# Kernel tuning notes

Hardware: AMD Instinct MI355X
Metric: run time of the kernel (lower is better)

## Reference

```python
import jax, jax.numpy as jnp
import numpy as np

HID = 128
CIN = 64


def _bilinear_up_align_corners(img, H, W):
    # torch F.interpolate(mode='bilinear', align_corners=True)
    b, c, h, w = img.shape
    ys = jnp.linspace(0.0, h - 1.0, H)
    xs = jnp.linspace(0.0, w - 1.0, W)
    y0 = jnp.floor(ys).astype(jnp.int32)
    y1 = jnp.minimum(y0 + 1, h - 1)
    wy = (ys - y0).astype(img.dtype)
    x0 = jnp.floor(xs).astype(jnp.int32)
    x1 = jnp.minimum(x0 + 1, w - 1)
    wx = (xs - x0).astype(img.dtype)
    rows = img[:, :, y0, :] * (1.0 - wy)[None, None, :, None] + img[:, :, y1, :] * wy[None, None, :, None]
    return rows[:, :, :, x0] * (1.0 - wx) + rows[:, :, :, x1] * wx


def _conv1x1(x, W, b):
    # 1x1 conv == channel-mixing GEMM: [B,C,H,W] x [O,C] -> [B,O,H,W]
    return jnp.einsum('bchw,oc->bohw', x, W) + b[None, :, None, None]


def _parallel_scan(feat, A_seq, B_seq, axis):
    # h_t = A_t h_{t-1} + B_t x_t  via cumprod/cumsum trick (with clamp, as in source)
    b = B_seq * feat
    P = jnp.cumprod(A_seq, axis=axis)
    P_safe = jnp.maximum(P, 1e-8)
    return P * jnp.cumsum(b / P_safe, axis=axis)


def setup_inputs() -> dict:
    key = jax.random.key(0)
    ks = jax.random.split(key, 12)
    inp = {
        'x': jax.random.normal(ks[0], (8, CIN, 128, 128), dtype=jnp.float32),
        'prior': jax.random.normal(ks[1], (8, 1, 64, 64), dtype=jnp.float32),
        'W_in': jax.random.normal(ks[2], (HID, CIN), dtype=jnp.float32) * 0.05,
        'b_in': jnp.zeros((HID,), dtype=jnp.float32),
        'W_out': jax.random.normal(ks[3], (CIN, HID), dtype=jnp.float32) * 0.05,
        'b_out': jnp.zeros((CIN,), dtype=jnp.float32),
        'W_delta': jax.random.normal(ks[4], (HID, HID), dtype=jnp.float32) * 0.05,
        'b_delta': jnp.zeros((HID,), dtype=jnp.float32),
        'W_B': jax.random.normal(ks[5], (HID, HID), dtype=jnp.float32) * 0.05,
        'b_B': jnp.zeros((HID,), dtype=jnp.float32),
        'lambda_delta': jnp.float32(0.1),
        'alpha': jnp.float32(0.1),
        'A': jax.random.normal(ks[6], (HID,), dtype=jnp.float32),
        'gamma': jnp.float32(0.0),
    }
    return inp


def reference(x, prior, W_in, b_in, W_out, b_out, W_delta, b_delta, W_B, b_B,
              lambda_delta, alpha, A, gamma):
    Bsz, C, H, W = x.shape
    prior_up = jnp.clip(_bilinear_up_align_corners(prior, H, W), -1.0, 1.0)
    x_proj = _conv1x1(x, W_in, b_in)                                   # [B,HID,H,W]
    delta = jax.nn.softplus(_conv1x1(x_proj, W_delta, b_delta) + lambda_delta * prior_up)
    B_k = _conv1x1(x_proj, W_B, b_B) * (1.0 + alpha * prior_up)
    A_neg = -jnp.exp(A)[None, :, None, None]                           # [1,HID,1,1]
    A_bar = jnp.exp(delta * A_neg)
    B_bar = delta * B_k
    scan_h = _parallel_scan(x_proj, A_bar, B_bar, axis=3)              # horizontal scan
    scan_v = _parallel_scan(x_proj, A_bar, B_bar, axis=2)              # vertical scan
    out = _conv1x1(scan_h + scan_v, W_out, b_out)
    return (x + gamma * out, prior_up)
```

## Files before the change

kernel.cpp:

```cpp
#include <hip/hip_runtime.h>
#include <math.h>

#define HID 128
#define CIN 64
#define NB 8
#define HD 128
#define WD 128
#define HW (HD*WD)

typedef float v2f __attribute__((ext_vector_type(2)));
typedef _Float16 h2 __attribute__((ext_vector_type(2)));
typedef _Float16 h4 __attribute__((ext_vector_type(4)));

#define WG_OFF   0
#define BD_OFF   24576
#define BB_OFF   24704
#define WO_OFF   24832

__global__ __launch_bounds__(256, 2) void head_kernel(const float* __restrict__ x,
                                                      const float* __restrict__ prior,
                                                      const float* __restrict__ W_in,
                                                      const float* __restrict__ b_in,
                                                      const float* __restrict__ W_out,
                                                      const float* __restrict__ W_delta,
                                                      const float* __restrict__ b_delta,
                                                      const float* __restrict__ W_B,
                                                      const float* __restrict__ b_B,
                                                      float* __restrict__ wcomp,
                                                      float* __restrict__ out0,
                                                      float* __restrict__ out1,
                                                      const float* __restrict__ gamma_p) {
    int bid = blockIdx.x;
    if (bid < 512) {
        int idx = bid * 256 + threadIdx.x;
        int b = idx >> 14;
        int rem = idx & 16383;
        int i = rem >> 7, j = rem & 127;
        const float scale = 63.0f / 127.0f;
        float ys = i * scale;
        float xs = j * scale;
        int y0 = (int)floorf(ys); int y1 = min(y0 + 1, 63);
        int x0 = (int)floorf(xs); int x1 = min(x0 + 1, 63);
        float wy = ys - (float)y0, wx = xs - (float)x0;
        const float* p = prior + b * 4096;
        float v00 = p[y0 * 64 + x0], v01 = p[y0 * 64 + x1];
        float v10 = p[y1 * 64 + x0], v11 = p[y1 * 64 + x1];
        float r0 = v00 * (1.f - wy) + v10 * wy;
        float r1 = v01 * (1.f - wy) + v11 * wy;
        float v = r0 * (1.f - wx) + r1 * wx;
        v = fminf(fmaxf(v, -1.f), 1.f);
        out1[idx] = v;
        return;
    }
    if (bid < 544) {
        int idx = (bid - 512) * 256 + threadIdx.x;
        int o = idx >> 6, c = idx & 63;
        float wd = 0.f, wb = 0.f;
        for (int h = 0; h < HID; ++h) {
            float wi = W_in[h * CIN + c];
            wd = fmaf(W_delta[o * HID + h], wi, wd);
            wb = fmaf(W_B[o * HID + h], wi, wb);
        }
        int og = o >> 4, j = o & 15;
        int base = WG_OFF + og * (CIN * 48) + c * 48;
        wcomp[base + j]      = W_in[o * CIN + c];
        wcomp[base + 16 + j] = wd;
        wcomp[base + 32 + j] = wb;
        return;
    }
    if (bid == 544) {
        int o = threadIdx.x;
        if (o < HID) {
            float sd = b_delta[o], sb = b_B[o];
            for (int h = 0; h < HID; ++h) {
                float bi = b_in[h];
                sd = fmaf(W_delta[o * HID + h], bi, sd);
                sb = fmaf(W_B[o * HID + h], bi, sb);
            }
            wcomp[BD_OFF + o] = sd;
            wcomp[BB_OFF + o] = sb;
        }
        return;
    }
    if (bid < 577) {
        int idx = (bid - 545) * 256 + threadIdx.x;
        int c = idx >> 6, o = idx & 63;
        wcomp[WO_OFF + idx] = W_out[o * HID + c];
        return;
    }
    if (gamma_p[0] != 0.f) return;
    int idx = ((bid - 577) * 256 + threadIdx.x) * 4;
    *(float4*)(out0 + idx) = *(const float4*)(x + idx);
    int idx2 = idx + 4194304;
    *(float4*)(out0 + idx2) = *(const float4*)(x + idx2);
}

__global__ __launch_bounds__(256, 2) void gate_kernel(const float* __restrict__ x,
                                                      const float* __restrict__ pu,
                                                      const float* __restrict__ wcomp,
                                                      const float* __restrict__ b_in,
                                                      const float* __restrict__ lam_p,
                                                      const float* __restrict__ alpha_p,
                                                      const float* __restrict__ A,
                                                      _Float16* __restrict__ Abar,
                                                      _Float16* __restrict__ bbuf,
                                                      const float* __restrict__ gamma_p) {
    if (gamma_p[0] == 0.f) return;
    const float lam = lam_p[0], alpha = alpha_p[0];
    int bx = blockIdx.x;
    int og = blockIdx.y;
    int b  = blockIdx.z;
    int p0 = bx * 1024 + threadIdx.x * 4;
    const float* wg = wcomp + WG_OFF + og * (CIN * 48);

    v2f ai[16][2], ad[16][2], ab[16][2];
#pragma unroll
    for (int j = 0; j < 16; ++j)
#pragma unroll
        for (int k = 0; k < 2; ++k) {
            ai[j][k] = (v2f){0.f, 0.f};
            ad[j][k] = (v2f){0.f, 0.f};
            ab[j][k] = (v2f){0.f, 0.f};
        }

    const float* xb = x + b * (CIN * HW) + p0;
    for (int c = 0; c < CIN; ++c) {
        float4 xv = *(const float4*)(xb + c * HW);
        v2f xlo = (v2f){xv.x, xv.y};
        v2f xhi = (v2f){xv.z, xv.w};
        const float* w = wg + c * 48;
#pragma unroll
        for (int j = 0; j < 16; ++j) {
            v2f wi = (v2f){w[j],      w[j]};
            v2f wd = (v2f){w[16 + j], w[16 + j]};
            v2f wb = (v2f){w[32 + j], w[32 + j]};
            ai[j][0] = __builtin_elementwise_fma(wi, xlo, ai[j][0]);
            ai[j][1] = __builtin_elementwise_fma(wi, xhi, ai[j][1]);
            ad[j][0] = __builtin_elementwise_fma(wd, xlo, ad[j][0]);
            ad[j][1] = __builtin_elementwise_fma(wd, xhi, ad[j][1]);
            ab[j][0] = __builtin_elementwise_fma(wb, xlo, ab[j][0]);
            ab[j][1] = __builtin_elementwise_fma(wb, xhi, ab[j][1]);
        }
    }

    float4 pu4 = *(const float4*)(pu + b * HW + p0);
    float pus[4] = {pu4.x, pu4.y, pu4.z, pu4.w};
    int base = b * (HID * HW) + p0;
#pragma unroll
    for (int j = 0; j < 16; ++j) {
        int o = og * 16 + j;
        float bi = b_in[o];
        float bd = wcomp[BD_OFF + o];
        float bb2 = wcomp[BB_OFF + o];
        float nA = -expf(A[o]);
        float adv[4] = {ad[j][0].x, ad[j][0].y, ad[j][1].x, ad[j][1].y};
        float aiv[4] = {ai[j][0].x, ai[j][0].y, ai[j][1].x, ai[j][1].y};
        float abv[4] = {ab[j][0].x, ab[j][0].y, ab[j][1].x, ab[j][1].y};
        float Ao[4], bo[4];
#pragma unroll
        for (int k = 0; k < 4; ++k) {
            float dv = adv[k] + bd + lam * pus[k];
            float d  = fmaxf(dv, 0.f) + log1pf(expf(-fabsf(dv)));
            Ao[k] = expf(d * nA);
            float feat = aiv[k] + bi;
            float Bk = (abv[k] + bb2) * (1.f + alpha * pus[k]);
            bo[k] = d * Bk * feat;
        }
        *(h4*)(Abar + base + o * HW) =
            (h4){(_Float16)Ao[0], (_Float16)Ao[1], (_Float16)Ao[2], (_Float16)Ao[3]};
        *(h4*)(bbuf + base + o * HW) =
            (h4){(_Float16)bo[0], (_Float16)bo[1], (_Float16)bo[2], (_Float16)bo[3]};
    }
}

__global__ __launch_bounds__(256) void vscan_kernel(const _Float16* __restrict__ Abar,
                                                    const _Float16* __restrict__ bbuf,
                                                    _Float16* __restrict__ vsum,
                                                    const float* __restrict__ gamma_p) {
    if (gamma_p[0] == 0.f) return;
    int idx = blockIdx.x * 256 + threadIdx.x;
    int base = (idx >> 7) * HW + (idx & 127);
    float P = 1.f, s = 0.f;
    for (int i = 0; i < HD; ++i) {
        int off = base + i * WD;
        float a  = (float)Abar[off];
        float bv = (float)bbuf[off];
        P *= a;
        s += bv / fmaxf(P, 1e-8f);
        vsum[off] = (_Float16)(P * s);
    }
}

__global__ __launch_bounds__(256, 2) void hconv_kernel(const _Float16* __restrict__ Abar,
                                                       const _Float16* __restrict__ bbuf,
                                                       const _Float16* __restrict__ vsum,
                                                       const float* __restrict__ x,
                                                       const float* __restrict__ wcomp,
                                                       const float* __restrict__ b_out,
                                                       const float* __restrict__ gamma_p,
                                                       float* __restrict__ out0) {
    float g = gamma_p[0];
    if (g == 0.f) return;
    __shared__ float slds[HID][WD];
    int row = blockIdx.x, b = blockIdx.y;
    int t = threadIdx.x, lane = t & 63, wv = t >> 6;
    const _Float16* Ab = Abar + (size_t)b * HID * HW + row * WD;
    const _Float16* Bb = bbuf + (size_t)b * HID * HW + row * WD;
    const _Float16* Vb = vsum + (size_t)b * HID * HW + row * WD;
    for (int it = 0; it < 32; ++it) {
        int c = wv * 32 + it;
        int coff = c * HW + lane * 2;
        h2 a2 = *(const h2*)(Ab + coff);
        h2 b2 = *(const h2*)(Bb + coff);
        float pa = (float)a2.x, pb0 = (float)a2.y;
        float bx0 = (float)b2.x, bx1 = (float)b2.y;
        float pb = pa * pb0;
        float Lp = pb;
#pragma unroll
        for (int off = 1; off < 64; off <<= 1) {
            float tt = __shfl_up(Lp, off, 64);
            if (lane >= off) Lp *= tt;
        }
        float ep = __shfl_up(Lp, 1, 64);
        if (lane == 0) ep = 1.f;
        float P0 = ep * pa, P1 = ep * pb;
        float q0 = bx0 / fmaxf(P0, 1e-8f);
        float q1 = bx1 / fmaxf(P1, 1e-8f);
        float s0 = q0, s1 = q0 + q1;
        float Ls = s1;
#pragma unroll
        for (int off = 1; off < 64; off <<= 1) {
            float tt = __shfl_up(Ls, off, 64);
            if (lane >= off) Ls += tt;
        }
        float es = __shfl_up(Ls, 1, 64);
        if (lane == 0) es = 0.f;
        float h0 = P0 * (es + s0), h1 = P1 * (es + s1);
        h2 v2 = *(const h2*)(Vb + coff);
        *(float2*)(&slds[c][lane * 2]) = make_float2(h0 + (float)v2.x, h1 + (float)v2.y);
    }
    __syncthreads();
    int wvu = __builtin_amdgcn_readfirstlane(wv);
    const float* wt = wcomp + WO_OFF;
    v2f acc[16];
#pragma unroll
    for (int j = 0; j < 16; ++j) acc[j] = (v2f){0.f, 0.f};
    for (int c = 0; c < HID; ++c) {
        v2f sv = *(const v2f*)(&slds[c][lane * 2]);
        const float* w = wt + c * 64 + wvu * 16;
#pragma unroll
        for (int j = 0; j < 16; ++j) {
            v2f wj = (v2f){w[j], w[j]};
            acc[j] = __builtin_elementwise_fma(wj, sv, acc[j]);
        }
    }
#pragma unroll
    for (int j = 0; j < 16; ++j) {
        int o = wvu * 16 + j;
        float bo = b_out[o];
        int oi = b * (CIN * HW) + o * HW + row * WD + lane * 2;
        float2 xv = *(const float2*)(x + oi);
        float2 o2;
        o2.x = xv.x + g * (acc[j].x + bo);
        o2.y = xv.y + g * (acc[j].y + bo);
        *(float2*)(out0 + oi) = o2;
    }
}

extern "C" void kernel_launch(void* const* d_in, const int* in_sizes, int n_in,
                              void* d_out, int out_size, void* d_ws, size_t ws_size,
                              hipStream_t stream) {
    const float* x       = (const float*)d_in[0];
    const float* prior   = (const float*)d_in[1];
    const float* W_in    = (const float*)d_in[2];
    const float* b_in    = (const float*)d_in[3];
    const float* W_out   = (const float*)d_in[4];
    const float* b_out   = (const float*)d_in[5];
    const float* W_delta = (const float*)d_in[6];
    const float* b_delta = (const float*)d_in[7];
    const float* W_B     = (const float*)d_in[8];
    const float* b_B     = (const float*)d_in[9];
    const float* lam     = (const float*)d_in[10];
    const float* alpha   = (const float*)d_in[11];
    const float* A       = (const float*)d_in[12];
    const float* gamma   = (const float*)d_in[13];

    float* out0 = (float*)d_out;
    float* out1 = (float*)d_out + NB * CIN * HW;

    const size_t FIELD = (size_t)NB * HID * HW;
    _Float16* Abar = (_Float16*)d_ws;
    _Float16* bbuf = Abar + FIELD;
    _Float16* vsum = bbuf + FIELD;
    float* wcomp   = (float*)(vsum + FIELD);

    head_kernel<<<dim3(4673), dim3(256), 0, stream>>>(
        x, prior, W_in, b_in, W_out, W_delta, b_delta, W_B, b_B, wcomp, out0, out1, gamma);
    gate_kernel<<<dim3(16, 8, NB), dim3(256), 0, stream>>>(
        x, out1, wcomp, b_in, lam, alpha, A, Abar, bbuf, gamma);
    vscan_kernel<<<dim3(512), dim3(256), 0, stream>>>(Abar, bbuf, vsum, gamma);
    hconv_kernel<<<dim3(HD, NB), dim3(256), 0, stream>>>(
        Abar, bbuf, vsum, x, wcomp, b_out, gamma, out0);
}
```

Measured before the change: 113.0 us.

## Fuse head kernel into gate kernel with per-block weight folding in LDS

Removes the separate head kernel. Each gate block now computes the bilinear upsample of the prior, folds W_delta/W_B with W_in for its 16 output channels into shared memory, and, when gamma is zero, copies its slice of x to the output. The hconv kernel reads W_out directly instead of a transposed copy. This saves a kernel launch and the workspace round trip, but every gate block redoes the weight-folding GEMM (128-deep loops) and W_out is now read with a strided access pattern.

```diff
diff --git a/kernel.cpp b/kernel.cpp
--- a/kernel.cpp
+++ b/kernel.cpp
@@ -12,106 +12,88 @@
 typedef _Float16 h2 __attribute__((ext_vector_type(2)));
 typedef _Float16 h4 __attribute__((ext_vector_type(4)));
 
-#define WG_OFF   0
-#define BD_OFF   24576
-#define BB_OFF   24704
-#define WO_OFF   24832
-
-__global__ __launch_bounds__(256, 2) void head_kernel(const float* __restrict__ x,
+__global__ __launch_bounds__(256, 2) void gate_kernel(const float* __restrict__ x,
                                                       const float* __restrict__ prior,
                                                       const float* __restrict__ W_in,
                                                       const float* __restrict__ b_in,
-                                                      const float* __restrict__ W_out,
                                                       const float* __restrict__ W_delta,
                                                       const float* __restrict__ b_delta,
                                                       const float* __restrict__ W_B,
                                                       const float* __restrict__ b_B,
-                                                      float* __restrict__ wcomp,
+                                                      const float* __restrict__ lam_p,
+                                                      const float* __restrict__ alpha_p,
+                                                      const float* __restrict__ A,
+                                                      const float* __restrict__ gamma_p,
+                                                      _Float16* __restrict__ Abar,
+                                                      _Float16* __restrict__ bbuf,
                                                       float* __restrict__ out0,
-                                                      float* __restrict__ out1,
-                                                      const float* __restrict__ gamma_p) {
-    int bid = blockIdx.x;
-    if (bid < 512) {
-        int idx = bid * 256 + threadIdx.x;
-        int b = idx >> 14;
-        int rem = idx & 16383;
-        int i = rem >> 7, j = rem & 127;
-        const float scale = 63.0f / 127.0f;
-        float ys = i * scale;
-        float xs = j * scale;
-        int y0 = (int)floorf(ys); int y1 = min(y0 + 1, 63);
+                                                      float* __restrict__ out1) {
+    __shared__ float sw[CIN][48];
+    __shared__ float sbd[16], sbb[16], snA[16], sbi[16];
+    const int bx = blockIdx.x, og = blockIdx.y, b = blockIdx.z;
+    const int tid = threadIdx.x;
+    const int p0 = bx * 1024 + tid * 4;
+    const float g = gamma_p[0];
+
+    const float scale = 63.0f / 127.0f;
+    int i = p0 >> 7;
+    float ys = i * scale;
+    int y0 = (int)floorf(ys); int y1 = min(y0 + 1, 63);
+    float wy = ys - (float)y0;
+    const float* pp = prior + b * 4096;
+    int col0 = p0 & 127;
+    float pus[4];
+#pragma unroll
+    for (int k = 0; k < 4; ++k) {
+        float xs = (col0 + k) * scale;
         int x0 = (int)floorf(xs); int x1 = min(x0 + 1, 63);
-        float wy = ys - (float)y0, wx = xs - (float)x0;
-        const float* p = prior + b * 4096;
-        float v00 = p[y0 * 64 + x0], v01 = p[y0 * 64 + x1];
-        float v10 = p[y1 * 64 + x0], v11 = p[y1 * 64 + x1];
+        float wx = xs - (float)x0;
+        float v00 = pp[y0 * 64 + x0], v01 = pp[y0 * 64 + x1];
+        float v10 = pp[y1 * 64 + x0], v11 = pp[y1 * 64 + x1];
         float r0 = v00 * (1.f - wy) + v10 * wy;
         float r1 = v01 * (1.f - wy) + v11 * wy;
         float v = r0 * (1.f - wx) + r1 * wx;
-        v = fminf(fmaxf(v, -1.f), 1.f);
-        out1[idx] = v;
+        pus[k] = fminf(fmaxf(v, -1.f), 1.f);
+    }
+    if (og == 0)
+        *(float4*)(out1 + b * HW + p0) = make_float4(pus[0], pus[1], pus[2], pus[3]);
+
+    if (g == 0.f) {
+        const float* xs0 = x + b * (CIN * HW) + (og * 8) * HW + p0;
+        float* o0 = out0 + b * (CIN * HW) + (og * 8) * HW + p0;
+#pragma unroll
+        for (int ch = 0; ch < 8; ++ch)
+            *(float4*)(o0 + ch * HW) = *(const float4*)(xs0 + ch * HW);
         return;
     }
-    if (bid < 544) {
-        int idx = (bid - 512) * 256 + threadIdx.x;
-        int o = idx >> 6, c = idx & 63;
+
+#pragma unroll
+    for (int k = 0; k < 4; ++k) {
+        int e = tid + k * 256;
+        int c = e >> 4, j = e & 15;
+        int o = og * 16 + j;
         float wd = 0.f, wb = 0.f;
         for (int h = 0; h < HID; ++h) {
             float wi = W_in[h * CIN + c];
             wd = fmaf(W_delta[o * HID + h], wi, wd);
             wb = fmaf(W_B[o * HID + h], wi, wb);
         }
-        int og = o >> 4, j = o & 15;
-        int base = WG_OFF + og * (CIN * 48) + c * 48;
-        wcomp[base + j]      = W_in[o * CIN + c];
-        wcomp[base + 16 + j] = wd;
-        wcomp[base + 32 + j] = wb;
-        return;
-    }
-    if (bid == 544) {
-        int o = threadIdx.x;
-        if (o < HID) {
-            float sd = b_delta[o], sb = b_B[o];
-            for (int h = 0; h < HID; ++h) {
-                float bi = b_in[h];
-                sd = fmaf(W_delta[o * HID + h], bi, sd);
-                sb = fmaf(W_B[o * HID + h], bi, sb);
-            }
-            wcomp[BD_OFF + o] = sd;
-            wcomp[BB_OFF + o] = sb;
-        }
-        return;
-    }
-    if (bid < 577) {
-        int idx = (bid - 545) * 256 + threadIdx.x;
-        int c = idx >> 6, o = idx & 63;
-        wcomp[WO_OFF + idx] = W_out[o * HID + c];
-        return;
-    }
-    if (gamma_p[0] != 0.f) return;
-    int idx = ((bid - 577) * 256 + threadIdx.x) * 4;
-    *(float4*)(out0 + idx) = *(const float4*)(x + idx);
-    int idx2 = idx + 4194304;
-    *(float4*)(out0 + idx2) = *(const float4*)(x + idx2);
-}
-
-__global__ __launch_bounds__(256, 2) void gate_kernel(const float* __restrict__ x,
-                                                      const float* __restrict__ pu,
-                                                      const float* __restrict__ wcomp,
-                                                      const float* __restrict__ b_in,
-                                                      const float* __restrict__ lam_p,
-                                                      const float* __restrict__ alpha_p,
-                                                      const float* __restrict__ A,
-                                                      _Float16* __restrict__ Abar,
-                                                      _Float16* __restrict__ bbuf,
-                                                      const float* __restrict__ gamma_p) {
-    if (gamma_p[0] == 0.f) return;
-    const float lam = lam_p[0], alpha = alpha_p[0];
-    int bx = blockIdx.x;
-    int og = blockIdx.y;
-    int b  = blockIdx.z;
-    int p0 = bx * 1024 + threadIdx.x * 4;
-    const float* wg = wcomp + WG_OFF + og * (CIN * 48);
+        sw[c][j]      = W_in[o * CIN + c];
+        sw[c][16 + j] = wd;
+        sw[c][32 + j] = wb;
+    }
+    if (tid < 16) {
+        int o = og * 16 + tid;
+        float sd = b_delta[o], sb = b_B[o];
+        for (int h = 0; h < HID; ++h) {
+            float bi = b_in[h];
+            sd = fmaf(W_delta[o * HID + h], bi, sd);
+            sb = fmaf(W_B[o * HID + h], bi, sb);
+        }
+        sbd[tid] = sd; sbb[tid] = sb;
+        snA[tid] = -expf(A[o]); sbi[tid] = b_in[o];
+    }
+    __syncthreads();
 
     v2f ai[16][2], ad[16][2], ab[16][2];
 #pragma unroll
@@ -128,7 +110,7 @@
         float4 xv = *(const float4*)(xb + c * HW);
         v2f xlo = (v2f){xv.x, xv.y};
         v2f xhi = (v2f){xv.z, xv.w};
-        const float* w = wg + c * 48;
+        const float* w = sw[c];
 #pragma unroll
         for (int j = 0; j < 16; ++j) {
             v2f wi = (v2f){w[j],      w[j]};
@@ -143,16 +125,12 @@
         }
     }
 
-    float4 pu4 = *(const float4*)(pu + b * HW + p0);
-    float pus[4] = {pu4.x, pu4.y, pu4.z, pu4.w};
+    const float lam = lam_p[0], alpha = alpha_p[0];
     int base = b * (HID * HW) + p0;
 #pragma unroll
     for (int j = 0; j < 16; ++j) {
         int o = og * 16 + j;
-        float bi = b_in[o];
-        float bd = wcomp[BD_OFF + o];
-        float bb2 = wcomp[BB_OFF + o];
-        float nA = -expf(A[o]);
+        float bi = sbi[j], bd = sbd[j], bb2 = sbb[j], nA = snA[j];
         float adv[4] = {ad[j][0].x, ad[j][0].y, ad[j][1].x, ad[j][1].y};
         float aiv[4] = {ai[j][0].x, ai[j][0].y, ai[j][1].x, ai[j][1].y};
         float abv[4] = {ab[j][0].x, ab[j][0].y, ab[j][1].x, ab[j][1].y};
@@ -195,7 +173,7 @@
                                                        const _Float16* __restrict__ bbuf,
                                                        const _Float16* __restrict__ vsum,
                                                        const float* __restrict__ x,
-                                                       const float* __restrict__ wcomp,
+                                                       const float* __restrict__ W_out,
                                                        const float* __restrict__ b_out,
                                                        const float* __restrict__ gamma_p,
                                                        float* __restrict__ out0) {
@@ -241,17 +219,17 @@
     }
     __syncthreads();
     int wvu = __builtin_amdgcn_readfirstlane(wv);
-    const float* wt = wcomp + WO_OFF;
+    const float* wrow = W_out + wvu * 16 * HID;
     v2f acc[16];
 #pragma unroll
     for (int j = 0; j < 16; ++j) acc[j] = (v2f){0.f, 0.f};
     for (int c = 0; c < HID; ++c) {
         v2f sv = *(const v2f*)(&slds[c][lane * 2]);
-        const float* w = wt + c * 64 + wvu * 16;
 #pragma unroll
         for (int j = 0; j < 16; ++j) {
-            v2f wj = (v2f){w[j], w[j]};
-            acc[j] = __builtin_elementwise_fma(wj, sv, acc[j]);
+            float wj = wrow[j * HID + c];
+            v2f w2 = (v2f){wj, wj};
+            acc[j] = __builtin_elementwise_fma(w2, sv, acc[j]);
         }
     }
 #pragma unroll
@@ -292,13 +270,11 @@
     _Float16* Abar = (_Float16*)d_ws;
     _Float16* bbuf = Abar + FIELD;
     _Float16* vsum = bbuf + FIELD;
-    float* wcomp   = (float*)(vsum + FIELD);
-
-    head_kernel<<<dim3(4673), dim3(256), 0, stream>>>(
-        x, prior, W_in, b_in, W_out, W_delta, b_delta, W_B, b_B, wcomp, out0, out1, gamma);
+
     gate_kernel<<<dim3(16, 8, NB), dim3(256), 0, stream>>>(
-        x, out1, wcomp, b_in, lam, alpha, A, Abar, bbuf, gamma);
+        x, prior, W_in, b_in, W_delta, b_delta, W_B, b_B,
+        lam, alpha, A, gamma, Abar, bbuf, out0, out1);
     vscan_kernel<<<dim3(512), dim3(256), 0, stream>>>(Abar, bbuf, vsum, gamma);
     hconv_kernel<<<dim3(HD, NB), dim3(256), 0, stream>>>(
-        Abar, bbuf, vsum, x, wcomp, b_out, gamma, out0);
-}
+        Abar, bbuf, vsum, x, W_out, b_out, gamma, out0);
+}
```

New measurement: 108.6 us. -3.8%, faster.
